# Kernel optimization log

Hardware: AMD Instinct MI355X
Metric: run time of the kernel (lower is better)

Reference implementation:

```python
import jax, jax.numpy as jnp
import numpy as np

C = 1024
N_HEADS = 16
HEAD_DIM = C // N_HEADS
D_FF = 4 * C
EPS = 1e-5


def setup_inputs() -> dict:
    key = jax.random.key(0)
    ks = jax.random.split(key, 6)
    B, T = 4, 2048
    x = jax.random.normal(ks[0], (B, T, C), dtype=jnp.float32)
    w_qkv = jax.random.normal(ks[1], (C, 3 * C), dtype=jnp.float32) * (C ** -0.5)
    w_proj = jax.random.normal(ks[2], (C, C), dtype=jnp.float32) * (C ** -0.5)
    w1 = jax.random.normal(ks[3], (C, D_FF), dtype=jnp.float32) * (C ** -0.5)
    b1 = jnp.zeros((D_FF,), dtype=jnp.float32)
    w2 = jax.random.normal(ks[4], (D_FF, C), dtype=jnp.float32) * (D_FF ** -0.5)
    b2 = jnp.zeros((C,), dtype=jnp.float32)
    ln1_g = jnp.ones((C,), dtype=jnp.float32)
    ln1_b = jnp.zeros((C,), dtype=jnp.float32)
    ln2_g = jnp.ones((C,), dtype=jnp.float32)
    ln2_b = jnp.zeros((C,), dtype=jnp.float32)
    return {"x": x, "ln1_g": ln1_g, "ln1_b": ln1_b, "ln2_g": ln2_g,
            "ln2_b": ln2_b, "w_qkv": w_qkv, "w_proj": w_proj,
            "w1": w1, "b1": b1, "w2": w2, "b2": b2}


def _layernorm(x, g, b):
    mu = jnp.mean(x, axis=-1, keepdims=True)
    var = jnp.mean(jnp.square(x - mu), axis=-1, keepdims=True)
    return (x - mu) * jax.lax.rsqrt(var + EPS) * g + b


def _attention(x, w_qkv, w_proj):
    B, T, Cdim = x.shape
    qkv = x @ w_qkv                                   # [B,T,3C]
    q, k, v = jnp.split(qkv, 3, axis=-1)
    # [B,T,C] -> [B,H,T,D]
    def heads(t):
        return t.reshape(B, T, N_HEADS, HEAD_DIM).transpose(0, 2, 1, 3)
    q, k, v = heads(q), heads(k), heads(v)
    scale = HEAD_DIM ** -0.5
    scores = jnp.einsum('bhqd,bhkd->bhqk', q, k) * scale  # [B,H,T,T]
    attn = jax.nn.softmax(scores, axis=-1)
    out = jnp.einsum('bhqk,bhkd->bhqd', attn, v)          # [B,H,T,D]
    out = out.transpose(0, 2, 1, 3).reshape(B, T, Cdim)
    return out @ w_proj


def reference(x, ln1_g, ln1_b, ln2_g, ln2_b, w_qkv, w_proj, w1, b1, w2, b2):
    x = x + _attention(_layernorm(x, ln1_g, ln1_b), w_qkv, w_proj)
    h = _layernorm(x, ln2_g, ln2_b)
    # exact (erf) GELU matches torch.nn.GELU default
    h = jax.nn.gelu(h @ w1 + b1, approximate=False) @ w2 + b2
    return x + h
```

## Files before the change

kernel.cpp:

```cpp
#include <hip/hip_runtime.h>
#include <hip/hip_bf16.h>
#include <math.h>

typedef __attribute__((ext_vector_type(8))) short bf16x8;
typedef __attribute__((ext_vector_type(4))) float f32x4;
typedef unsigned short ushort_t;

__device__ __forceinline__ ushort_t f2bf(float f) {
    union { float f; unsigned u; } v; v.f = f;
    unsigned r = v.u + 0x7FFF + ((v.u >> 16) & 1);
    return (ushort_t)(r >> 16);
}

__device__ __forceinline__ unsigned pack2bf(float a, float b) {
    union { float f; unsigned u; } x, y; x.f = a; y.f = b;
    return __builtin_amdgcn_perm(y.u + 0x8000u, x.u + 0x8000u, 0x07060302u);
}

__device__ __forceinline__ unsigned cvtpk2bf(float a, float b) {
    unsigned r;
    asm("v_cvt_pk_bf16_f32 %0, %1, %2" : "=v"(r) : "v"(a), "v"(b));
    return r;
}

__device__ __forceinline__ void gl2lds(const void* g, void* l) {
    __builtin_amdgcn_global_load_lds(
        (const __attribute__((address_space(1))) void*)g,
        (__attribute__((address_space(3))) void*)l, 16, 0, 0);
}

__device__ __forceinline__ float fast_gelu(float tt) {
    float t2 = tt * tt;
    float arg = tt * fmaf(0.07135481283f, t2, 1.595769122f);
    float e = __builtin_amdgcn_exp2f(arg * -1.442695041f);
    return tt * __builtin_amdgcn_rcpf(1.0f + e);
}

__global__ __launch_bounds__(256)
void tcast_all(const float* __restrict__ wqkv, const float* __restrict__ wproj,
               const float* __restrict__ w1, const float* __restrict__ w2,
               ushort_t* __restrict__ wqkvT, ushort_t* __restrict__ wprojT,
               ushort_t* __restrict__ w1T, ushort_t* __restrict__ w2T,
               float qscale) {
    __shared__ float tile[32][33];
    int id = blockIdx.x;
    const float* in; ushort_t* out; int R, Cc, gx, scale_n;
    if (id < 3072)      { in = wqkv;  out = wqkvT;  R = 1024; Cc = 3072; gx = 96;  scale_n = 1024; }
    else if (id < 4096) { id -= 3072; in = wproj; out = wprojT; R = 1024; Cc = 1024; gx = 32; scale_n = 0; }
    else if (id < 8192) { id -= 4096; in = w1;    out = w1T;    R = 1024; Cc = 4096; gx = 128; scale_n = 0; }
    else                { id -= 8192; in = w2;    out = w2T;    R = 4096; Cc = 1024; gx = 32; scale_n = 0; }
    int bc = (id % gx) * 32, br = (id / gx) * 32;
    int tx = threadIdx.x, ty = threadIdx.y;
    #pragma unroll
    for (int i = 0; i < 32; i += 8)
        tile[ty + i][tx] = in[(size_t)(br + ty + i) * Cc + bc + tx];
    __syncthreads();
    #pragma unroll
    for (int i = 0; i < 32; i += 8) {
        int n = bc + ty + i;
        float v = tile[tx][ty + i];
        if (n < scale_n) v *= qscale;
        out[(size_t)n * R + br + tx] = f2bf(v);
    }
}

__global__ __launch_bounds__(256)
void ln_kernel(const float* __restrict__ x, const float* __restrict__ g,
               const float* __restrict__ b, ushort_t* __restrict__ out) {
    const int row = blockIdx.x;
    const int t = threadIdx.x;
    const float4 xv = ((const float4*)(x + (size_t)row * 1024))[t];
    float s  = xv.x + xv.y + xv.z + xv.w;
    float ss = xv.x*xv.x + xv.y*xv.y + xv.z*xv.z + xv.w*xv.w;
    #pragma unroll
    for (int off = 32; off > 0; off >>= 1) {
        s  += __shfl_xor(s, off);
        ss += __shfl_xor(ss, off);
    }
    __shared__ float red[8];
    int wave = t >> 6, lane = t & 63;
    if (lane == 0) { red[wave] = s; red[4 + wave] = ss; }
    __syncthreads();
    s  = red[0] + red[1] + red[2] + red[3];
    ss = red[4] + red[5] + red[6] + red[7];
    float mu  = s * (1.0f / 1024.0f);
    float var = ss * (1.0f / 1024.0f) - mu * mu;
    float rstd = rsqrtf(var + 1e-5f);
    float4 gv = ((const float4*)g)[t];
    float4 bv = ((const float4*)b)[t];
    ushort4 o;
    o.x = f2bf((xv.x - mu) * rstd * gv.x + bv.x);
    o.y = f2bf((xv.y - mu) * rstd * gv.y + bv.y);
    o.z = f2bf((xv.z - mu) * rstd * gv.z + bv.z);
    o.w = f2bf((xv.w - mu) * rstd * gv.w + bv.w);
    ((ushort4*)(out + (size_t)row * 1024))[t] = o;
}

template<int MODE, int K, int N>
__global__ __launch_bounds__(256)
void gemm_bt(const ushort_t* __restrict__ A, const ushort_t* __restrict__ Bt,
             void* __restrict__ Cout, const float* __restrict__ bias,
             const float* __restrict__ res, ushort_t* __restrict__ vTout) {
    constexpr int BK = 64;
    __shared__ __align__(16) ushort_t As[128 * 64];
    __shared__ __align__(16) ushort_t Bs[128 * 64];
    const int tid = threadIdx.x;
    const int wave = tid >> 6, lane = tid & 63;
    const int quad = lane >> 4, l16 = lane & 15;
    const int m0 = blockIdx.y * 128, n0 = blockIdx.x * 128;
    const int wm = (wave >> 1) * 64, wn = (wave & 1) * 64;

    const int r0 = tid >> 3, pc = tid & 7;
    const int lc = pc ^ (r0 & 7);
    const ushort_t* aSrc = A  + (size_t)(m0 + r0) * K + lc * 8;
    const ushort_t* bSrc = Bt + (size_t)(n0 + r0) * K + lc * 8;
    char* aDst = (char*)As + wave * 1024;
    char* bDst = (char*)Bs + wave * 1024;
    const int swz = l16 & 7;

    f32x4 acc[4][4] = {};

    for (int k0 = 0; k0 < K; k0 += BK) {
        __syncthreads();
        #pragma unroll
        for (int c = 0; c < 4; ++c) {
            gl2lds(aSrc + (size_t)c * 32 * K + k0, aDst + c * 4096);
            gl2lds(bSrc + (size_t)c * 32 * K + k0, bDst + c * 4096);
        }
        __syncthreads();
        #pragma unroll
        for (int ks = 0; ks < 2; ++ks) {
            const int cko = ((ks * 4 + quad) ^ swz) * 8;
            bf16x8 af[4], bfr[4];
            #pragma unroll
            for (int i = 0; i < 4; ++i)
                af[i] = *(const bf16x8*)(&As[(wm + i * 16 + l16) * 64 + cko]);
            #pragma unroll
            for (int j = 0; j < 4; ++j)
                bfr[j] = *(const bf16x8*)(&Bs[(wn + j * 16 + l16) * 64 + cko]);
            #pragma unroll
            for (int i = 0; i < 4; ++i)
                #pragma unroll
                for (int j = 0; j < 4; ++j)
                    acc[i][j] = __builtin_amdgcn_mfma_f32_16x16x32_bf16(
                        af[i], bfr[j], acc[i][j], 0, 0, 0);
        }
    }

    if constexpr (MODE == 0) {
        if (vTout && n0 >= 2048) {
            #pragma unroll
            for (int i = 0; i < 4; ++i) {
                int m = m0 + wm + i * 16 + quad * 4;
                int bb = m >> 11, t = m & 2047;
                #pragma unroll
                for (int j = 0; j < 4; ++j) {
                    int nn = n0 - 2048 + wn + j * 16 + l16;
                    int h = nn >> 6, d = nn & 63;
                    uint2 pk;
                    pk.x = pack2bf(acc[i][j][0], acc[i][j][1]);
                    pk.y = pack2bf(acc[i][j][2], acc[i][j][3]);
                    *(uint2*)(vTout + ((size_t)(bb * 16 + h) * 64 + d) * 2048 + t) = pk;
                }
            }
            return;
        }
    }
    float bj[4];
    if constexpr (MODE == 2 || MODE == 3) {
        #pragma unroll
        for (int j = 0; j < 4; ++j) bj[j] = bias[n0 + wn + j * 16 + l16];
    }
    #pragma unroll
    for (int i = 0; i < 4; ++i) {
        #pragma unroll
        for (int j = 0; j < 4; ++j) {
            #pragma unroll
            for (int r = 0; r < 4; ++r) {
                int m = m0 + wm + i * 16 + quad * 4 + r;
                int n = n0 + wn + j * 16 + l16;
                size_t idx = (size_t)m * N + n;
                float v = acc[i][j][r];
                if constexpr (MODE == 0) {
                    ((ushort_t*)Cout)[idx] = f2bf(v);
                } else if constexpr (MODE == 1) {
                    ((float*)Cout)[idx] = v + res[idx];
                } else if constexpr (MODE == 2) {
                    ((ushort_t*)Cout)[idx] = f2bf(fast_gelu(v + bj[j]));
                } else {
                    ((float*)Cout)[idx] = v + bj[j] + res[idx];
                }
            }
        }
    }
}

__global__ __launch_bounds__(256)
void attn_kernel(const ushort_t* __restrict__ qkv, const ushort_t* __restrict__ vT,
                 ushort_t* __restrict__ out) {
    constexpr int T = 2048, C3 = 3072, BQ = 128;
    __shared__ __align__(16) ushort_t Ks[2][64 * 64];
    __shared__ __align__(16) ushort_t Vs[2][64 * 64];
    const int bh = blockIdx.x, b = bh >> 4, h = bh & 15;
    const int qt = blockIdx.y;
    const int tid = threadIdx.x, wave = tid >> 6, lane = tid & 63;
    const int quad = lane >> 4, l16 = lane & 15;
    const int swz = l16 & 7;

    bf16x8 qf[2][2];
    {
        const ushort_t* Qg = qkv + ((size_t)b * T + qt * BQ + wave * 32) * C3 + h * 64;
        #pragma unroll
        for (int i = 0; i < 2; ++i)
            #pragma unroll
            for (int ks = 0; ks < 2; ++ks)
                qf[i][ks] = *(const bf16x8*)(Qg + (size_t)(i * 16 + l16) * C3 + ks * 32 + quad * 8);
    }
    bf16x8 onesf;
    #pragma unroll
    for (int e = 0; e < 8; ++e) onesf[e] = (short)0x3F80;

    const int r0 = tid >> 3, pc = tid & 7;
    const int lc = pc ^ (r0 & 7);
    const ushort_t* KgB = qkv + (size_t)b * T * C3 + 1024 + h * 64 + (size_t)r0 * C3 + lc * 8;
    const ushort_t* VgB = vT + (size_t)bh * 64 * T + (size_t)r0 * T + lc * 8;
    char* kDst0 = (char*)&Ks[0][0] + wave * 1024;
    char* vDst0 = (char*)&Vs[0][0] + wave * 1024;

    f32x4 o_acc[2][4] = {};
    f32x4 l_acc[2] = {};

    #pragma unroll
    for (int c = 0; c < 2; ++c) {
        gl2lds(KgB + (size_t)c * 32 * C3, kDst0 + c * 4096);
        gl2lds(VgB + (size_t)c * 32 * T,  vDst0 + c * 4096);
    }

    for (int kt = 0; kt < T / 64; ++kt) {
        const int cur = kt & 1;
        __syncthreads();
        if (kt + 1 < T / 64) {
            const int nb = (cur ^ 1) * 8192;
            #pragma unroll
            for (int c = 0; c < 2; ++c) {
                gl2lds(KgB + ((size_t)(kt + 1) * 64 + c * 32) * C3, kDst0 + nb + c * 4096);
                gl2lds(VgB + (size_t)c * 32 * T + (kt + 1) * 64,    vDst0 + nb + c * 4096);
            }
        }
        const ushort_t* Kc = &Ks[cur][0];
        const ushort_t* Vc = &Vs[cur][0];

        #pragma unroll
        for (int i = 0; i < 2; ++i) {
            f32x4 s1[4] = {};
            #pragma unroll
            for (int ks = 0; ks < 2; ++ks) {
                const int cko = ((ks * 4 + quad) ^ swz) * 8;
                bf16x8 kf[4];
                #pragma unroll
                for (int j = 0; j < 4; ++j)
                    kf[j] = *(const bf16x8*)(&Kc[(j * 16 + l16) * 64 + cko]);
                __builtin_amdgcn_s_setprio(1);
                #pragma unroll
                for (int j = 0; j < 4; ++j)
                    s1[j] = __builtin_amdgcn_mfma_f32_16x16x32_bf16(
                        kf[j], qf[i][ks], s1[j], 0, 0, 0);
                __builtin_amdgcn_s_setprio(0);
            }

            unsigned u[4][2];
            #pragma unroll
            for (int j = 0; j < 4; ++j) {
                float p0 = __builtin_amdgcn_exp2f(s1[j][0]);
                float p1 = __builtin_amdgcn_exp2f(s1[j][1]);
                float p2 = __builtin_amdgcn_exp2f(s1[j][2]);
                float p3 = __builtin_amdgcn_exp2f(s1[j][3]);
                u[j][0] = cvtpk2bf(p0, p1);
                u[j][1] = cvtpk2bf(p2, p3);
            }
            bf16x8 pfi[2];
            #pragma unroll
            for (int ks2 = 0; ks2 < 2; ++ks2) {
                unsigned d0 = u[2 * ks2][0], d2 = u[2 * ks2 + 1][0];
                asm("v_permlane32_swap_b32 %0, %1\n\t"
                    "v_permlane16_swap_b32 %0, %1" : "+v"(d0), "+v"(d2));
                unsigned d1 = u[2 * ks2][1], d3 = u[2 * ks2 + 1][1];
                asm("v_permlane32_swap_b32 %0, %1\n\t"
                    "v_permlane16_swap_b32 %0, %1" : "+v"(d1), "+v"(d3));
                union { unsigned d[4]; bf16x8 v; } fr;
                fr.d[0] = d0; fr.d[1] = d1; fr.d[2] = d2; fr.d[3] = d3;
                pfi[ks2] = fr.v;
            }

            #pragma unroll
            for (int ks2 = 0; ks2 < 2; ++ks2) {
                const int cko = ((ks2 * 4 + quad) ^ swz) * 8;
                bf16x8 vf[4];
                #pragma unroll
                for (int j = 0; j < 4; ++j)
                    vf[j] = *(const bf16x8*)(&Vc[(j * 16 + l16) * 64 + cko]);
                __builtin_amdgcn_s_setprio(1);
                #pragma unroll
                for (int j = 0; j < 4; ++j)
                    o_acc[i][j] = __builtin_amdgcn_mfma_f32_16x16x32_bf16(
                        pfi[ks2], vf[j], o_acc[i][j], 0, 0, 0);
                l_acc[i] = __builtin_amdgcn_mfma_f32_16x16x32_bf16(
                    pfi[ks2], onesf, l_acc[i], 0, 0, 0);
                __builtin_amdgcn_s_setprio(0);
            }
        }
    }

    #pragma unroll
    for (int i = 0; i < 2; ++i) {
        #pragma unroll
        for (int r = 0; r < 4; ++r) {
            float inv = 1.0f / l_acc[i][r];
            int row = qt * BQ + wave * 32 + i * 16 + quad * 4 + r;
            size_t orow = ((size_t)b * T + row) * 1024 + h * 64;
            #pragma unroll
            for (int j = 0; j < 4; ++j)
                out[orow + j * 16 + l16] = f2bf(o_acc[i][j][r] * inv);
        }
    }
}

extern "C" void kernel_launch(void* const* d_in, const int* in_sizes, int n_in,
                              void* d_out, int out_size, void* d_ws, size_t ws_size,
                              hipStream_t stream) {
    const float* x     = (const float*)d_in[0];
    const float* ln1g  = (const float*)d_in[1];
    const float* ln1b  = (const float*)d_in[2];
    const float* ln2g  = (const float*)d_in[3];
    const float* ln2b  = (const float*)d_in[4];
    const float* wqkv  = (const float*)d_in[5];
    const float* wproj = (const float*)d_in[6];
    const float* w1    = (const float*)d_in[7];
    const float* b1    = (const float*)d_in[8];
    const float* w2    = (const float*)d_in[9];
    const float* b2    = (const float*)d_in[10];
    float* out = (float*)d_out;

    const size_t MT = 8192;
    ushort_t* wqkvT  = (ushort_t*)d_ws;
    ushort_t* wprojT = wqkvT  + (size_t)3072 * 1024;
    ushort_t* w1T    = wprojT + (size_t)1024 * 1024;
    ushort_t* w2T    = w1T    + (size_t)4096 * 1024;
    ushort_t* xn     = w2T    + (size_t)1024 * 4096;
    ushort_t* qkvb   = xn     + MT * 1024;
    ushort_t* attnb  = qkvb   + MT * 3072;
    float*    x2     = (float*)(attnb + MT * 1024);
    ushort_t* xn2    = (ushort_t*)(x2 + MT * 1024);
    ushort_t* h1     = xn;
    ushort_t* vT     = (ushort_t*)x2;

    dim3 blk256(256);
    dim3 tblk(32, 8);
    const float qscale = 0.125f * 1.4426950408889634f;

    tcast_all<<<dim3(12288), tblk, 0, stream>>>(wqkv, wproj, w1, w2,
                                                wqkvT, wprojT, w1T, w2T, qscale);

    ln_kernel<<<dim3(8192), blk256, 0, stream>>>(x, ln1g, ln1b, xn);
    gemm_bt<0, 1024, 3072><<<dim3(24, 64), blk256, 0, stream>>>(xn, wqkvT, qkvb, nullptr, nullptr, vT);
    attn_kernel<<<dim3(64, 16), blk256, 0, stream>>>(qkvb, vT, attnb);
    gemm_bt<1, 1024, 1024><<<dim3(8, 64), blk256, 0, stream>>>(attnb, wprojT, x2, nullptr, x, nullptr);
    ln_kernel<<<dim3(8192), blk256, 0, stream>>>(x2, ln2g, ln2b, xn2);
    gemm_bt<2, 1024, 4096><<<dim3(32, 64), blk256, 0, stream>>>(xn2, w1T, h1, b1, nullptr, nullptr);
    gemm_bt<3, 4096, 1024><<<dim3(8, 64), blk256, 0, stream>>>(h1, w2T, out, b2, x2, nullptr);
}
```

Before: 503.7 us.

## Add 256x256-tile 8-wave GEMM kernel for QKV and FFN1 projections

Adds a new GEMM kernel with 256x256 output tiles, 512 threads, double-buffered LDS filled by direct global-to-LDS loads, and prefetches spread across the MFMA sub-phases. It also remaps block IDs for L2 locality and raises wave priority around the MFMA runs. The QKV and FFN-up GEMMs now use it, which cuts global and LDS traffic per FLOP compared with the 128-tile kernel. In exchange it uses more LDS (128KB) and registers, and with fewer workgroups the GPU may be less evenly filled.

```diff
diff --git a/kernel.cpp b/kernel.cpp
--- a/kernel.cpp
+++ b/kernel.cpp
@@ -147,25 +147,6 @@
         }
     }
 
-    if constexpr (MODE == 0) {
-        if (vTout && n0 >= 2048) {
-            #pragma unroll
-            for (int i = 0; i < 4; ++i) {
-                int m = m0 + wm + i * 16 + quad * 4;
-                int bb = m >> 11, t = m & 2047;
-                #pragma unroll
-                for (int j = 0; j < 4; ++j) {
-                    int nn = n0 - 2048 + wn + j * 16 + l16;
-                    int h = nn >> 6, d = nn & 63;
-                    uint2 pk;
-                    pk.x = pack2bf(acc[i][j][0], acc[i][j][1]);
-                    pk.y = pack2bf(acc[i][j][2], acc[i][j][3]);
-                    *(uint2*)(vTout + ((size_t)(bb * 16 + h) * 64 + d) * 2048 + t) = pk;
-                }
-            }
-            return;
-        }
-    }
     float bj[4];
     if constexpr (MODE == 2 || MODE == 3) {
         #pragma unroll
@@ -189,6 +170,136 @@
                     ((ushort_t*)Cout)[idx] = f2bf(fast_gelu(v + bj[j]));
                 } else {
                     ((float*)Cout)[idx] = v + bj[j] + res[idx];
+                }
+            }
+        }
+    }
+}
+
+template<int MODE, int K, int N>
+__global__ __launch_bounds__(512, 2)
+void gemm256(const ushort_t* __restrict__ A, const ushort_t* __restrict__ Bt,
+             void* __restrict__ Cout, const float* __restrict__ bias,
+             ushort_t* __restrict__ vTout) {
+    constexpr int BK = 64;
+    constexpr int NT = K / BK;
+    __shared__ __align__(16) ushort_t As[2][256 * 64];
+    __shared__ __align__(16) ushort_t Bs[2][256 * 64];
+    const int tid = threadIdx.x;
+    const int wave = tid >> 6, lane = tid & 63;
+    const int quad = lane >> 4, l16 = lane & 15;
+    const int nwg = gridDim.x * gridDim.y;
+    int id = blockIdx.y * gridDim.x + blockIdx.x;
+    id = (id & 7) * (nwg >> 3) + (id >> 3);
+    const int m0 = (id / gridDim.x) * 256, n0 = (id % gridDim.x) * 256;
+    const int wm = (wave >> 2) * 128, wn = (wave & 3) * 64;
+
+    const int r0 = tid >> 3, pc = tid & 7;
+    const int lc = pc ^ (r0 & 7);
+    const ushort_t* aSrc = A  + (size_t)(m0 + r0) * K + lc * 8;
+    const ushort_t* bSrc = Bt + (size_t)(n0 + r0) * K + lc * 8;
+    const int swz = l16 & 7;
+
+    f32x4 acc[8][4] = {};
+
+    #pragma unroll
+    for (int c = 0; c < 4; ++c) {
+        gl2lds(aSrc + (size_t)c * 64 * K, (char*)&As[0][0] + c * 8192 + wave * 1024);
+        gl2lds(bSrc + (size_t)c * 64 * K, (char*)&Bs[0][0] + c * 8192 + wave * 1024);
+    }
+    __syncthreads();
+
+    for (int t = 0; t < NT; ++t) {
+        const int cur = t & 1;
+        const ushort_t* Ac = &As[cur][0];
+        const ushort_t* Bc = &Bs[cur][0];
+        char* aD = (char*)&As[cur ^ 1][0] + wave * 1024;
+        char* bD = (char*)&Bs[cur ^ 1][0] + wave * 1024;
+        const size_t koff = (size_t)(t + 1) * BK;
+        const bool pre = (t + 1 < NT);
+
+        bf16x8 bfr[4][2];
+        #pragma unroll
+        for (int p = 0; p < 4; ++p) {
+            if (p == 0) {
+                #pragma unroll
+                for (int j = 0; j < 4; ++j)
+                    #pragma unroll
+                    for (int ks = 0; ks < 2; ++ks)
+                        bfr[j][ks] = *(const bf16x8*)(
+                            &Bc[(wn + j * 16 + l16) * 64 + ((ks * 4 + quad) ^ swz) * 8]);
+            }
+            bf16x8 af[2][2];
+            #pragma unroll
+            for (int di = 0; di < 2; ++di)
+                #pragma unroll
+                for (int ks = 0; ks < 2; ++ks)
+                    af[di][ks] = *(const bf16x8*)(
+                        &Ac[(wm + (p * 2 + di) * 16 + l16) * 64 + ((ks * 4 + quad) ^ swz) * 8]);
+            if (pre) {
+                if (p < 2) {
+                    gl2lds(aSrc + koff + (size_t)(p * 2) * 64 * K,     aD + (p * 2) * 8192);
+                    gl2lds(aSrc + koff + (size_t)(p * 2 + 1) * 64 * K, aD + (p * 2 + 1) * 8192);
+                } else {
+                    gl2lds(bSrc + koff + (size_t)((p - 2) * 2) * 64 * K,     bD + ((p - 2) * 2) * 8192);
+                    gl2lds(bSrc + koff + (size_t)((p - 2) * 2 + 1) * 64 * K, bD + ((p - 2) * 2 + 1) * 8192);
+                }
+            }
+            __builtin_amdgcn_s_barrier();
+            __builtin_amdgcn_s_setprio(1);
+            #pragma unroll
+            for (int ks = 0; ks < 2; ++ks)
+                #pragma unroll
+                for (int di = 0; di < 2; ++di)
+                    #pragma unroll
+                    for (int j = 0; j < 4; ++j)
+                        acc[p * 2 + di][j] = __builtin_amdgcn_mfma_f32_16x16x32_bf16(
+                            af[di][ks], bfr[j][ks], acc[p * 2 + di][j], 0, 0, 0);
+            __builtin_amdgcn_s_setprio(0);
+            __builtin_amdgcn_s_barrier();
+        }
+        asm volatile("s_waitcnt vmcnt(0)" ::: "memory");
+        __builtin_amdgcn_s_barrier();
+    }
+
+    if constexpr (MODE == 0) {
+        if (vTout && n0 >= 2048) {
+            #pragma unroll
+            for (int i = 0; i < 8; ++i) {
+                int m = m0 + wm + i * 16 + quad * 4;
+                int bb = m >> 11, t = m & 2047;
+                #pragma unroll
+                for (int j = 0; j < 4; ++j) {
+                    int nn = n0 - 2048 + wn + j * 16 + l16;
+                    int h = nn >> 6, d = nn & 63;
+                    uint2 pk;
+                    pk.x = pack2bf(acc[i][j][0], acc[i][j][1]);
+                    pk.y = pack2bf(acc[i][j][2], acc[i][j][3]);
+                    *(uint2*)(vTout + ((size_t)(bb * 16 + h) * 64 + d) * 2048 + t) = pk;
+                }
+            }
+            return;
+        }
+    }
+    float bj[4];
+    if constexpr (MODE == 2) {
+        #pragma unroll
+        for (int j = 0; j < 4; ++j) bj[j] = bias[n0 + wn + j * 16 + l16];
+    }
+    #pragma unroll
+    for (int i = 0; i < 8; ++i) {
+        #pragma unroll
+        for (int j = 0; j < 4; ++j) {
+            #pragma unroll
+            for (int r = 0; r < 4; ++r) {
+                int m = m0 + wm + i * 16 + quad * 4 + r;
+                int n = n0 + wn + j * 16 + l16;
+                size_t idx = (size_t)m * N + n;
+                float v = acc[i][j][r];
+                if constexpr (MODE == 0) {
+                    ((ushort_t*)Cout)[idx] = f2bf(v);
+                } else if constexpr (MODE == 2) {
+                    ((ushort_t*)Cout)[idx] = f2bf(fast_gelu(v + bj[j]));
                 }
             }
         }
@@ -355,6 +466,7 @@
     ushort_t* vT     = (ushort_t*)x2;
 
     dim3 blk256(256);
+    dim3 blk512(512);
     dim3 tblk(32, 8);
     const float qscale = 0.125f * 1.4426950408889634f;
 
@@ -362,10 +474,10 @@
                                                 wqkvT, wprojT, w1T, w2T, qscale);
 
     ln_kernel<<<dim3(8192), blk256, 0, stream>>>(x, ln1g, ln1b, xn);
-    gemm_bt<0, 1024, 3072><<<dim3(24, 64), blk256, 0, stream>>>(xn, wqkvT, qkvb, nullptr, nullptr, vT);
+    gemm256<0, 1024, 3072><<<dim3(12, 32), blk512, 0, stream>>>(xn, wqkvT, qkvb, nullptr, vT);
     attn_kernel<<<dim3(64, 16), blk256, 0, stream>>>(qkvb, vT, attnb);
     gemm_bt<1, 1024, 1024><<<dim3(8, 64), blk256, 0, stream>>>(attnb, wprojT, x2, nullptr, x, nullptr);
     ln_kernel<<<dim3(8192), blk256, 0, stream>>>(x2, ln2g, ln2b, xn2);
-    gemm_bt<2, 1024, 4096><<<dim3(32, 64), blk256, 0, stream>>>(xn2, w1T, h1, b1, nullptr, nullptr);
+    gemm256<2, 1024, 4096><<<dim3(16, 32), blk512, 0, stream>>>(xn2, w1T, h1, b1, nullptr);
     gemm_bt<3, 4096, 1024><<<dim3(8, 64), blk256, 0, stream>>>(h1, w2T, out, b2, x2, nullptr);
 }
```

Result: slower. 536.1 us (+6.4%).
